# Kernel optimization log

Measured on AMD Instinct MI355X. Metric: run time of the kernel, lower is better.

## Reference

```python
import jax, jax.numpy as jnp
import numpy as np

B, L, D, DP = 64, 4096, 512, 64


def setup_inputs() -> dict:
    key = jax.random.key(0)
    ks = jax.random.split(key, 7)
    s = 0.02
    return {
        "source": jax.random.normal(ks[0], (B, D), jnp.float32),
        "main_embs": jax.random.normal(ks[1], (L, B, D), jnp.float32),   # time-major memory bank
        "pos_embs": jax.random.normal(ks[2], (L, B, DP), jnp.float32),
        "W_main_in": jax.random.normal(ks[3], (D, D), jnp.float32) * s,  # main_scorer.linear_in (no bias)
        "W_pos_in": jax.random.normal(ks[4], (D, DP), jnp.float32) * s,  # pos_scorer.linear_in (no bias)
        "W_out": jax.random.normal(ks[5], (D, 2 * D), jnp.float32) * s,  # linear_out (no bias, attn_type!='mlp')
        "memory_lengths": jnp.maximum(jax.random.randint(ks[6], (B,), 1, L + 1), 1),
    }


def reference(source, main_embs, pos_embs, W_main_in, W_pos_in, W_out, memory_lengths):
    # to batch-major: (B, L, D) / (B, L, DP)
    me = jnp.transpose(main_embs, (1, 0, 2))
    pe = jnp.transpose(pos_embs, (1, 0, 2))

    # 'general' scorer: project context then dot with query (qrs_len == 1)
    mc = jnp.einsum("bld,ed->ble", me, W_main_in)          # (B, L, D)
    main_align = jnp.einsum("bd,bld->bl", source, mc)      # (B, L)
    pc = jnp.einsum("blp,dp->bld", pe, W_pos_in)           # (B, L, D)
    pos_align = jnp.einsum("bd,bld->bl", source, pc)       # (B, L)

    # length mask + softmax on each branch
    mask = jnp.arange(me.shape[1])[None, :] < memory_lengths[:, None]  # (B, L)
    neg_inf = jnp.float32(-jnp.inf)
    ma = jax.nn.softmax(jnp.where(mask, main_align, neg_inf), axis=-1)
    pa = jax.nn.softmax(jnp.where(mask, pos_align, neg_inf), axis=-1)

    # elementwise combine + renormalize
    av = ma * pa
    av = av / jnp.sum(av, axis=-1, keepdims=True)

    # context vector + output projection + tanh
    c_t = jnp.einsum("bl,bld->bd", av, me)                 # (B, D)
    concat_c = jnp.concatenate([c_t, source], axis=-1)     # (B, 2D)
    attn_h = jnp.tanh(concat_c @ W_out.T)                  # (B, D)

    return attn_h, av, ma, pa
```

## Files before the change

kernel.cpp:

```cpp
#include <hip/hip_runtime.h>
#include <cstddef>

#define NB 64
#define NL 4096
#define ND 512
#define NDP 64
#define LC 64
#define NLC (NL / LC)

typedef float v2f __attribute__((ext_vector_type(2)));

__device__ __forceinline__ v2f fma2(v2f a, v2f b, v2f c) {
    return __builtin_elementwise_fma(a, b, c);
}

__global__ void __launch_bounds__(128) queries_kernel(
    const float* __restrict__ source, const float* __restrict__ Wmi,
    const float* __restrict__ Wpi, float* __restrict__ qpm,
    float* __restrict__ qpp)
{
    __shared__ float s[128];
    const int b  = blockIdx.x >> 2;
    const int eq = blockIdx.x & 3;
    const int t  = threadIdx.x;
    const int e0 = eq * 128;
    s[t] = source[b * ND + e0 + t];
    __syncthreads();

    const int d0 = t * 4;
    float4 a0 = {0,0,0,0}, a1 = {0,0,0,0};
    #pragma unroll 4
    for (int e = 0; e < 128; e += 2) {
        const float4 w0 = *(const float4*)(Wmi + (size_t)(e0 + e) * ND + d0);
        const float4 w1 = *(const float4*)(Wmi + (size_t)(e0 + e + 1) * ND + d0);
        const float x0 = s[e], x1 = s[e + 1];
        a0.x = fmaf(x0, w0.x, a0.x); a0.y = fmaf(x0, w0.y, a0.y);
        a0.z = fmaf(x0, w0.z, a0.z); a0.w = fmaf(x0, w0.w, a0.w);
        a1.x = fmaf(x1, w1.x, a1.x); a1.y = fmaf(x1, w1.y, a1.y);
        a1.z = fmaf(x1, w1.z, a1.z); a1.w = fmaf(x1, w1.w, a1.w);
    }
    a0.x += a1.x; a0.y += a1.y; a0.z += a1.z; a0.w += a1.w;
    *(float4*)(qpm + (size_t)(b * 4 + eq) * ND + d0) = a0;

    if (t < NDP) {
        float c0 = 0.f, c1 = 0.f;
        #pragma unroll 4
        for (int e = 0; e < 128; e += 2) {
            c0 = fmaf(s[e],     Wpi[(size_t)(e0 + e) * NDP + t],     c0);
            c1 = fmaf(s[e + 1], Wpi[(size_t)(e0 + e + 1) * NDP + t], c1);
        }
        qpp[(b * 4 + eq) * NDP + t] = c0 + c1;
    }
}

__global__ void __launch_bounds__(256) pass1_kernel(
    const float* __restrict__ me, const float* __restrict__ pe,
    const float* __restrict__ qpm, const float* __restrict__ qpp,
    const int* __restrict__ mem_len,
    float* __restrict__ a_main, float* __restrict__ a_pos,
    float* __restrict__ Sbuf, float* __restrict__ MZ)
{
    __shared__ __align__(16) float qp_lds[4][NDP];
    const int lane = threadIdx.x & 63;
    const int wid  = threadIdx.x >> 6;
    const int bg   = blockIdx.x & 15;
    const int lc   = blockIdx.x >> 4;
    const int b    = (((bg + (lc >> 4)) & 15) << 2) | wid;

    const int len = mem_len[b];
    const int l0  = lc * LC;
    if (l0 >= len) return;
    const int nrow = min(LC, len - l0);

    float4 q0 = {0,0,0,0}, q1 = {0,0,0,0};
    float qp = 0.f;
    #pragma unroll
    for (int eq = 0; eq < 4; ++eq) {
        const float4* qr = (const float4*)(qpm + (size_t)(b * 4 + eq) * ND);
        const float4 u0 = qr[lane], u1 = qr[64 + lane];
        q0.x += u0.x; q0.y += u0.y; q0.z += u0.z; q0.w += u0.w;
        q1.x += u1.x; q1.y += u1.y; q1.z += u1.z; q1.w += u1.w;
        qp += qpp[(b * 4 + eq) * NDP + lane];
    }
    qp_lds[wid][lane] = qp;

    float accp = 0.f;
    {
        const float4* pr = (const float4*)(pe + ((size_t)(l0 + lane) * NB + b) * NDP);
        #pragma unroll
        for (int k = 0; k < 16; ++k) {
            const float4 pv = pr[k];
            const float4 qv = *(const float4*)&qp_lds[wid][k * 4];
            accp = fmaf(pv.x, qv.x, accp);
            accp = fmaf(pv.y, qv.y, accp);
            accp = fmaf(pv.z, qv.z, accp);
            accp = fmaf(pv.w, qv.w, accp);
        }
        if (lane < nrow) a_pos[(size_t)b * NL + l0 + lane] = accp;
    }
    const int accp_i = __float_as_int(accp);

    const size_t rstride = (size_t)NB * ND;
    const float* rp = me + ((size_t)l0 * NB + b) * ND;
    float4 c0 = ((const float4*)rp)[lane];
    float4 c1 = ((const float4*)rp)[64 + lane];

    float m = -1e30f, Z = 0.f, keep = 0.f;
    v2f S0 = {0,0}, S1 = {0,0}, S2 = {0,0}, S3 = {0,0};

    for (int i = 0; i < nrow; ++i) {
        const float* np = rp + ((i + 1 < nrow) ? rstride : 0);
        const float4 n0 = ((const float4*)np)[lane];
        const float4 n1 = ((const float4*)np)[64 + lane];

        v2f d2 = {0.f, 0.f};
        d2 = fma2((v2f){c0.x, c0.y}, (v2f){q0.x, q0.y}, d2);
        d2 = fma2((v2f){c0.z, c0.w}, (v2f){q0.z, q0.w}, d2);
        d2 = fma2((v2f){c1.x, c1.y}, (v2f){q1.x, q1.y}, d2);
        d2 = fma2((v2f){c1.z, c1.w}, (v2f){q1.z, q1.w}, d2);
        float accm = d2.x + d2.y;
        #pragma unroll
        for (int off = 32; off; off >>= 1)
            accm += __shfl_xor(accm, off);

        keep = (lane == i) ? accm : keep;
        const float ap = __int_as_float(__builtin_amdgcn_readlane(accp_i, i));
        const float sv = accm + ap;

        if (sv > m) {
            const float sc = __expf(m - sv);
            const v2f sc2 = {sc, sc};
            Z = fmaf(Z, sc, 1.f);
            S0 = fma2(S0, sc2, (v2f){c0.x, c0.y});
            S1 = fma2(S1, sc2, (v2f){c0.z, c0.w});
            S2 = fma2(S2, sc2, (v2f){c1.x, c1.y});
            S3 = fma2(S3, sc2, (v2f){c1.z, c1.w});
            m = sv;
        } else {
            const float w = __expf(sv - m);
            const v2f w2 = {w, w};
            Z += w;
            S0 = fma2((v2f){c0.x, c0.y}, w2, S0);
            S1 = fma2((v2f){c0.z, c0.w}, w2, S1);
            S2 = fma2((v2f){c1.x, c1.y}, w2, S2);
            S3 = fma2((v2f){c1.z, c1.w}, w2, S3);
        }
        c0 = n0; c1 = n1;
        rp += rstride;
    }

    if (lane < nrow) a_main[(size_t)b * NL + l0 + lane] = keep;

    float* sp = Sbuf + ((size_t)b * NLC + lc) * ND;
    ((float4*)sp)[lane]      = (float4){S0.x, S0.y, S1.x, S1.y};
    ((float4*)sp)[64 + lane] = (float4){S2.x, S2.y, S3.x, S3.y};
    if (lane == 0) {
        MZ[2 * (b * NLC + lc)]     = m;
        MZ[2 * (b * NLC + lc) + 1] = Z;
    }
}

__global__ void __launch_bounds__(1024) stats_finalize_kernel(
    const float* __restrict__ MZ, const int* __restrict__ mem_len,
    float* __restrict__ ma_io, float* __restrict__ pa_io,
    float* __restrict__ out_av, float* __restrict__ coef)
{
    __shared__ float red[16][6];
    __shared__ float bc[6];
    const int b = blockIdx.x;
    const int tid = threadIdx.x;
    const int lane = tid & 63, wid = tid >> 6;
    const int len = mem_len[b];

    float va[4], vp[4];
    float Am = -1e30f, Pm = -1e30f, Cm = -1e30f;
    #pragma unroll
    for (int k = 0; k < 4; ++k) {
        const int l = tid + k * 1024;
        va[k] = ma_io[(size_t)b * NL + l];
        vp[k] = pa_io[(size_t)b * NL + l];
        if (l < len) {
            Am = fmaxf(Am, va[k]);
            Pm = fmaxf(Pm, vp[k]);
            Cm = fmaxf(Cm, va[k] + vp[k]);
        }
    }
    #pragma unroll
    for (int off = 32; off; off >>= 1) {
        Am = fmaxf(Am, __shfl_xor(Am, off));
        Pm = fmaxf(Pm, __shfl_xor(Pm, off));
        Cm = fmaxf(Cm, __shfl_xor(Cm, off));
    }
    if (lane == 0) { red[wid][0] = Am; red[wid][1] = Pm; red[wid][2] = Cm; }
    __syncthreads();
    if (tid < 16) {
        float a = red[tid][0], p = red[tid][1], c = red[tid][2];
        #pragma unroll
        for (int off = 8; off; off >>= 1) {
            a = fmaxf(a, __shfl_xor(a, off));
            p = fmaxf(p, __shfl_xor(p, off));
            c = fmaxf(c, __shfl_xor(c, off));
        }
        if (tid == 0) { bc[0] = a; bc[1] = p; bc[2] = c; }
    }
    __syncthreads();
    const float MA = bc[0], MP = bc[1], MC = bc[2];

    float Az = 0.f, Pz = 0.f, Cz = 0.f;
    #pragma unroll
    for (int k = 0; k < 4; ++k) {
        const int l = tid + k * 1024;
        if (l < len) {
            Az += __expf(va[k] - MA);
            Pz += __expf(vp[k] - MP);
            Cz += __expf(va[k] + vp[k] - MC);
        }
    }
    #pragma unroll
    for (int off = 32; off; off >>= 1) {
        Az += __shfl_xor(Az, off);
        Pz += __shfl_xor(Pz, off);
        Cz += __shfl_xor(Cz, off);
    }
    if (lane == 0) { red[wid][3] = Az; red[wid][4] = Pz; red[wid][5] = Cz; }
    __syncthreads();
    if (tid < 16) {
        float a = red[tid][3], p = red[tid][4], c = red[tid][5];
        #pragma unroll
        for (int off = 8; off; off >>= 1) {
            a += __shfl_xor(a, off);
            p += __shfl_xor(p, off);
            c += __shfl_xor(c, off);
        }
        if (tid == 0) { bc[3] = a; bc[4] = p; bc[5] = c; }
    }
    __syncthreads();
    const float iA = 1.f / bc[3], iP = 1.f / bc[4], iC = 1.f / bc[5];

    if (tid < NLC) {
        const int nv = (len + LC - 1) >> 6;
        const float mlc = MZ[2 * (b * NLC + tid)];
        coef[b * NLC + tid] = (tid < nv) ? __expf(mlc - MC) * iC : 0.f;
    }

    #pragma unroll
    for (int k = 0; k < 4; ++k) {
        const int l = tid + k * 1024;
        const bool v = l < len;
        const size_t idx = (size_t)b * NL + l;
        ma_io[idx]  = v ? __expf(va[k] - MA) * iA : 0.f;
        pa_io[idx]  = v ? __expf(vp[k] - MP) * iP : 0.f;
        out_av[idx] = v ? __expf(va[k] + vp[k] - MC) * iC : 0.f;
    }
}

__global__ void __launch_bounds__(256) ctx_kernel(
    const float* __restrict__ Sbuf, const float* __restrict__ coef,
    const int* __restrict__ mem_len, float* __restrict__ c_t)
{
    __shared__ float sh[3][64];
    const int b = blockIdx.x >> 3, dseg = blockIdx.x & 7;
    const int dl = threadIdx.x & 63, k = threadIdx.x >> 6;
    const int d = dseg * 64 + dl;
    const int nv = (mem_len[b] + LC - 1) >> 6;
    float acc = 0.f;
    for (int lcc = k; lcc < nv; lcc += 4)
        acc = fmaf(coef[b * NLC + lcc],
                   Sbuf[((size_t)b * NLC + lcc) * ND + d], acc);
    if (k) sh[k - 1][dl] = acc;
    __syncthreads();
    if (k == 0)
        c_t[b * ND + d] = acc + sh[0][dl] + sh[1][dl] + sh[2][dl];
}

__global__ void __launch_bounds__(256) out_kernel(
    const float* __restrict__ c_t, const float* __restrict__ source,
    const float* __restrict__ Wout, float* __restrict__ attn_h)
{
    __shared__ float cs[2 * ND];
    const int b = blockIdx.x >> 3;
    const int eg = blockIdx.x & 7;
    const int tid = threadIdx.x;

    for (int d = tid; d < ND; d += 256) {
        cs[d] = c_t[b * ND + d];
        cs[ND + d] = source[b * ND + d];
    }
    __syncthreads();

    const int wid = tid >> 6, lane = tid & 63;
    const float4* csv = (const float4*)cs;
    for (int e = eg * 64 + wid; e < eg * 64 + 64; e += 4) {
        const float4* wrow = (const float4*)(Wout + (size_t)e * 2 * ND);
        float acc = 0.f;
        #pragma unroll
        for (int j = 0; j < 4; ++j) {
            const float4 w = wrow[lane + 64 * j];
            const float4 c = csv[lane + 64 * j];
            acc += w.x * c.x + w.y * c.y + w.z * c.z + w.w * c.w;
        }
        #pragma unroll
        for (int off = 32; off; off >>= 1) acc += __shfl_xor(acc, off);
        if (lane == 0) attn_h[(size_t)b * ND + e] = tanhf(acc);
    }
}

extern "C" void kernel_launch(void* const* d_in, const int* in_sizes, int n_in,
                              void* d_out, int out_size, void* d_ws, size_t ws_size,
                              hipStream_t stream)
{
    const float* source = (const float*)d_in[0];
    const float* me     = (const float*)d_in[1];
    const float* pe     = (const float*)d_in[2];
    const float* Wmi    = (const float*)d_in[3];
    const float* Wpi    = (const float*)d_in[4];
    const float* Wout   = (const float*)d_in[5];
    const int*   lens   = (const int*)d_in[6];

    float* out    = (float*)d_out;
    float* attn_h = out;
    float* av     = attn_h + NB * ND;
    float* ma     = av + NB * NL;
    float* pa     = ma + NB * NL;

    float* ws    = (float*)d_ws;
    float* qpm   = ws;
    float* qpp   = qpm + NB * 4 * ND;
    float* Sbuf  = qpp + NB * 4 * NDP;
    float* MZ    = Sbuf + (size_t)NB * NLC * ND;
    float* coef  = MZ + NB * NLC * 2;
    float* c_t   = coef + NB * NLC;

    queries_kernel        <<<NB * 4, 128, 0, stream>>>(source, Wmi, Wpi, qpm, qpp);
    pass1_kernel          <<<NLC * 16, 256, 0, stream>>>(me, pe, qpm, qpp, lens,
                                                         ma, pa, Sbuf, MZ);
    stats_finalize_kernel <<<NB, 1024, 0, stream>>>(MZ, lens, ma, pa, av, coef);
    ctx_kernel            <<<NB * 8, 256, 0, stream>>>(Sbuf, coef, lens, c_t);
    out_kernel            <<<NB * 8, 256, 0, stream>>>(c_t, source, Wout, attn_h);
}
```

Baseline: 111.3 us.

## Compact live (batch, chunk) tasks into a work table and deepen row prefetch

```diff
diff --git a/kernel.cpp b/kernel.cpp
--- a/kernel.cpp
+++ b/kernel.cpp
@@ -7,6 +7,7 @@
 #define NDP 64
 #define LC 64
 #define NLC (NL / LC)
+#define NSLOT 4096
 
 typedef float v2f __attribute__((ext_vector_type(2)));
 
@@ -14,11 +15,30 @@
     return __builtin_elementwise_fma(a, b, c);
 }
 
-__global__ void __launch_bounds__(128) queries_kernel(
+__global__ void __launch_bounds__(128) queries_plan_kernel(
     const float* __restrict__ source, const float* __restrict__ Wmi,
-    const float* __restrict__ Wpi, float* __restrict__ qpm,
-    float* __restrict__ qpp)
-{
+    const float* __restrict__ Wpi, const int* __restrict__ lens,
+    float* __restrict__ qpm, float* __restrict__ qpp,
+    int* __restrict__ table)
+{
+    if (blockIdx.x == NB * 4) {
+        if (threadIdx.x < 64) {
+            const int lane = threadIdx.x;
+            const int nc = (lens[lane] + LC - 1) >> 6;
+            int pre = nc;
+            #pragma unroll
+            for (int off = 1; off < 64; off <<= 1) {
+                const int v = __shfl_up(pre, off);
+                if (lane >= off) pre += v;
+            }
+            const int start = pre - nc;
+            for (int j = 0; j < nc; ++j) table[start + j] = (lane << 6) | j;
+            const int T = __shfl(pre, 63);
+            for (int s = T + lane; s < NSLOT; s += 64) table[s] = -1;
+        }
+        return;
+    }
+
     __shared__ float s[128];
     const int b  = blockIdx.x >> 2;
     const int eq = blockIdx.x & 3;
@@ -56,20 +76,20 @@
 __global__ void __launch_bounds__(256) pass1_kernel(
     const float* __restrict__ me, const float* __restrict__ pe,
     const float* __restrict__ qpm, const float* __restrict__ qpp,
-    const int* __restrict__ mem_len,
+    const int* __restrict__ mem_len, const int* __restrict__ table,
     float* __restrict__ a_main, float* __restrict__ a_pos,
     float* __restrict__ Sbuf, float* __restrict__ MZ)
 {
     __shared__ __align__(16) float qp_lds[4][NDP];
     const int lane = threadIdx.x & 63;
     const int wid  = threadIdx.x >> 6;
-    const int bg   = blockIdx.x & 15;
-    const int lc   = blockIdx.x >> 4;
-    const int b    = (((bg + (lc >> 4)) & 15) << 2) | wid;
-
-    const int len = mem_len[b];
-    const int l0  = lc * LC;
-    if (l0 >= len) return;
+    const int task = table[blockIdx.x * 4 + wid];
+    if (task < 0) return;
+    const int b  = task >> 6;
+    const int lc = task & 63;
+
+    const int len  = mem_len[b];
+    const int l0   = lc * LC;
     const int nrow = min(LC, len - l0);
 
     float4 q0 = {0,0,0,0}, q1 = {0,0,0,0};
@@ -102,23 +122,26 @@
 
     const size_t rstride = (size_t)NB * ND;
     const float* rp = me + ((size_t)l0 * NB + b) * ND;
+    const float* rp1 = rp + ((nrow > 1) ? rstride : 0);
     float4 c0 = ((const float4*)rp)[lane];
     float4 c1 = ((const float4*)rp)[64 + lane];
+    float4 d0 = ((const float4*)rp1)[lane];
+    float4 d1 = ((const float4*)rp1)[64 + lane];
 
     float m = -1e30f, Z = 0.f, keep = 0.f;
     v2f S0 = {0,0}, S1 = {0,0}, S2 = {0,0}, S3 = {0,0};
 
     for (int i = 0; i < nrow; ++i) {
-        const float* np = rp + ((i + 1 < nrow) ? rstride : 0);
+        const float* np = rp + ((i + 2 < nrow) ? 2 * rstride : 0);
         const float4 n0 = ((const float4*)np)[lane];
         const float4 n1 = ((const float4*)np)[64 + lane];
 
-        v2f d2 = {0.f, 0.f};
-        d2 = fma2((v2f){c0.x, c0.y}, (v2f){q0.x, q0.y}, d2);
-        d2 = fma2((v2f){c0.z, c0.w}, (v2f){q0.z, q0.w}, d2);
-        d2 = fma2((v2f){c1.x, c1.y}, (v2f){q1.x, q1.y}, d2);
-        d2 = fma2((v2f){c1.z, c1.w}, (v2f){q1.z, q1.w}, d2);
-        float accm = d2.x + d2.y;
+        v2f dd = {0.f, 0.f};
+        dd = fma2((v2f){c0.x, c0.y}, (v2f){q0.x, q0.y}, dd);
+        dd = fma2((v2f){c0.z, c0.w}, (v2f){q0.z, q0.w}, dd);
+        dd = fma2((v2f){c1.x, c1.y}, (v2f){q1.x, q1.y}, dd);
+        dd = fma2((v2f){c1.z, c1.w}, (v2f){q1.z, q1.w}, dd);
+        float accm = dd.x + dd.y;
         #pragma unroll
         for (int off = 32; off; off >>= 1)
             accm += __shfl_xor(accm, off);
@@ -145,7 +168,7 @@
             S2 = fma2((v2f){c1.x, c1.y}, w2, S2);
             S3 = fma2((v2f){c1.z, c1.w}, w2, S3);
         }
-        c0 = n0; c1 = n1;
+        c0 = d0; c1 = d1; d0 = n0; d1 = n1;
         rp += rstride;
     }
 
@@ -330,10 +353,12 @@
     float* MZ    = Sbuf + (size_t)NB * NLC * ND;
     float* coef  = MZ + NB * NLC * 2;
     float* c_t   = coef + NB * NLC;
-
-    queries_kernel        <<<NB * 4, 128, 0, stream>>>(source, Wmi, Wpi, qpm, qpp);
-    pass1_kernel          <<<NLC * 16, 256, 0, stream>>>(me, pe, qpm, qpp, lens,
-                                                         ma, pa, Sbuf, MZ);
+    int*   table = (int*)(c_t + NB * ND);
+
+    queries_plan_kernel   <<<NB * 4 + 1, 128, 0, stream>>>(source, Wmi, Wpi,
+                                                           lens, qpm, qpp, table);
+    pass1_kernel          <<<NSLOT / 4, 256, 0, stream>>>(me, pe, qpm, qpp, lens,
+                                                          table, ma, pa, Sbuf, MZ);
     stats_finalize_kernel <<<NB, 1024, 0, stream>>>(MZ, lens, ma, pa, av, coef);
     ctx_kernel            <<<NB * 8, 256, 0, stream>>>(Sbuf, coef, lens, c_t);
     out_kernel            <<<NB * 8, 256, 0, stream>>>(c_t, source, Wout, attn_h);
```

Result: slower. 115.2 us (+3.4%).
